# Optimization experiments

Hardware: AMD Instinct MI355X
Metric: run time of the kernel (lower is better)

Reference implementation:

```python
import jax, jax.numpy as jnp
import numpy as np

BETA = 0.0  # vcon_steps=0 -> beta=0 -> pure MAM (max+min) path


def setup_inputs() -> dict:
    key = jax.random.key(0)
    k1, k2, k3 = jax.random.split(key, 3)
    in_features, out_features, tokens = 1024, 512, 256
    x = jax.random.normal(k1, (tokens, in_features), dtype=jnp.float32)
    # torch stores weight as [out_features, in_features]
    weight = jax.random.normal(k2, (out_features, in_features), dtype=jnp.float32) * (1.0 / np.sqrt(in_features))
    bias = jax.random.normal(k3, (out_features,), dtype=jnp.float32) * 0.02
    return {"x": x, "weight": weight, "bias": bias}


def reference(x, weight, bias):
    # w: [K, N] as in the kernel (weight.T)
    w = weight.T
    # elementwise-product tensor [B, K, N]; kernel fuses this with online max/min
    prod = x[:, :, None] * w[None, :, :]
    mam = jnp.max(prod, axis=1) + jnp.min(prod, axis=1)  # [B, N]
    if BETA > 0.0:
        lin = jnp.matmul(x, w)
        out = BETA * lin + (1.0 - BETA) * mam + bias
    else:
        out = mam + bias
    return out
```

## Files before the change

kernel.cpp:

```cpp
#include <hip/hip_runtime.h>
#include <float.h>

#define B_TOK 256
#define N_OUT 512
#define K_IN  1024

#define KSPLIT 8
#define KT     (K_IN / KSPLIT)
#define BT     16
#define NT     64

__global__ __launch_bounds__(256)
void mam_stage1(const float* __restrict__ x, const float* __restrict__ w,
                float* __restrict__ pmx, float* __restrict__ pmn) {
    __shared__ float lds[10240];
    float* ws = lds;
    float* xs = lds + 8192;

    const int tid = threadIdx.x;
    const int wv  = tid >> 6;
    const int ln  = tid & 63;
    const int b0  = blockIdx.x * BT;
    const int n0  = blockIdx.y * NT;
    const int kc  = blockIdx.z * KT;

    {
        const int cb = ln & 15;
        const int u  = ln >> 4;
#pragma unroll
        for (int p = 0; p < 4; ++p) {
            const int r = 16 * wv + 4 * p + u;
            const int q = r >> 2;
            const float* src = w + (size_t)(n0 + r) * K_IN + kc;
#pragma unroll
            for (int m = 0; m < 2; ++m) {
                const int c = cb + 16 * m;
                const float4 v = *reinterpret_cast<const float4*>(src + c * 4);
                *reinterpret_cast<float4*>(&ws[r * 128 + ((c ^ q) << 2)]) = v;
            }
        }
    }
    {
        const int cb = ln & 15;
        const int u  = ln >> 4;
        const int b  = 4 * wv + u;
        const float* src = x + (size_t)(b0 + b) * K_IN + kc;
#pragma unroll
        for (int m = 0; m < 2; ++m) {
            const int c = cb + 16 * m;
            const float4 v = *reinterpret_cast<const float4*>(src + c * 4);
            *reinterpret_cast<float4*>(&xs[b * 128 + ((c ^ b) << 2)]) = v;
        }
    }
    __syncthreads();

    const int nq = ln & 15;
    const int bq = ln >> 4;

    float mx[4][4], mn[4][4];
#pragma unroll
    for (int i = 0; i < 4; ++i)
#pragma unroll
        for (int j = 0; j < 4; ++j) { mx[i][j] = -FLT_MAX; mn[i][j] = FLT_MAX; }

#pragma unroll 2
    for (int cl = 0; cl < 8; ++cl) {
        const int c = 8 * wv + cl;
        float4 wf[4], xf[4];
#pragma unroll
        for (int j = 0; j < 4; ++j)
            wf[j] = *reinterpret_cast<const float4*>(
                &ws[(4 * nq + j) * 128 + ((c ^ nq) << 2)]);
#pragma unroll
        for (int i = 0; i < 4; ++i)
            xf[i] = *reinterpret_cast<const float4*>(
                &xs[(4 * bq + i) * 128 + ((c ^ (4 * bq + i)) << 2)]);

#pragma unroll
        for (int i = 0; i < 4; ++i) {
#pragma unroll
            for (int j = 0; j < 4; ++j) {
                const float p0 = xf[i].x * wf[j].x;
                const float p1 = xf[i].y * wf[j].y;
                const float p2 = xf[i].z * wf[j].z;
                const float p3 = xf[i].w * wf[j].w;
                mx[i][j] = fmaxf(fmaxf(mx[i][j], p0), p1);
                mx[i][j] = fmaxf(fmaxf(mx[i][j], p2), p3);
                mn[i][j] = fminf(fminf(mn[i][j], p0), p1);
                mn[i][j] = fminf(fminf(mn[i][j], p2), p3);
            }
        }
    }

    __syncthreads();
    float* red = lds;
#pragma unroll
    for (int i = 0; i < 4; ++i) {
        const int ol = (4 * bq + i) * 64 + 4 * nq;
        float4 a = make_float4(mx[i][0], mx[i][1], mx[i][2], mx[i][3]);
        float4 d = make_float4(mn[i][0], mn[i][1], mn[i][2], mn[i][3]);
        *reinterpret_cast<float4*>(&red[(wv * 2 + 0) * 1024 + ol]) = a;
        *reinterpret_cast<float4*>(&red[(wv * 2 + 1) * 1024 + ol]) = d;
    }
    __syncthreads();

    {
        float4 MX = *reinterpret_cast<const float4*>(&red[0 * 1024 + tid * 4]);
        float4 MN = *reinterpret_cast<const float4*>(&red[1 * 1024 + tid * 4]);
#pragma unroll
        for (int v = 1; v < 4; ++v) {
            const float4 a = *reinterpret_cast<const float4*>(&red[(v * 2 + 0) * 1024 + tid * 4]);
            const float4 d = *reinterpret_cast<const float4*>(&red[(v * 2 + 1) * 1024 + tid * 4]);
            MX.x = fmaxf(MX.x, a.x); MX.y = fmaxf(MX.y, a.y);
            MX.z = fmaxf(MX.z, a.z); MX.w = fmaxf(MX.w, a.w);
            MN.x = fminf(MN.x, d.x); MN.y = fminf(MN.y, d.y);
            MN.z = fminf(MN.z, d.z); MN.w = fminf(MN.w, d.w);
        }
        const int bl = tid >> 4;
        const int nl = (tid & 15) * 4;
        const size_t o = ((size_t)blockIdx.z * B_TOK + b0 + bl) * N_OUT + n0 + nl;
        *reinterpret_cast<float4*>(&pmx[o]) = MX;
        *reinterpret_cast<float4*>(&pmn[o]) = MN;
    }
}

__global__ __launch_bounds__(256)
void mam_stage2(const float* __restrict__ pmx, const float* __restrict__ pmn,
                const float* __restrict__ bias, float* __restrict__ out) {
    const size_t i4 = ((size_t)blockIdx.x * 256 + threadIdx.x) * 4;
    const size_t plane = (size_t)B_TOK * N_OUT;
    float4 MX = *reinterpret_cast<const float4*>(pmx + i4);
    float4 MN = *reinterpret_cast<const float4*>(pmn + i4);
#pragma unroll
    for (int p = 1; p < KSPLIT; ++p) {
        const float4 a = *reinterpret_cast<const float4*>(pmx + (size_t)p * plane + i4);
        const float4 d = *reinterpret_cast<const float4*>(pmn + (size_t)p * plane + i4);
        MX.x = fmaxf(MX.x, a.x); MX.y = fmaxf(MX.y, a.y);
        MX.z = fmaxf(MX.z, a.z); MX.w = fmaxf(MX.w, a.w);
        MN.x = fminf(MN.x, d.x); MN.y = fminf(MN.y, d.y);
        MN.z = fminf(MN.z, d.z); MN.w = fminf(MN.w, d.w);
    }
    const float4 bb = *reinterpret_cast<const float4*>(bias + (i4 & (N_OUT - 1)));
    float4 o;
    o.x = MX.x + MN.x + bb.x; o.y = MX.y + MN.y + bb.y;
    o.z = MX.z + MN.z + bb.z; o.w = MX.w + MN.w + bb.w;
    *reinterpret_cast<float4*>(out + i4) = o;
}

__global__ __launch_bounds__(256)
void mam_simple(const float* __restrict__ x, const float* __restrict__ w,
                const float* __restrict__ bias, float* __restrict__ out) {
    const int idx = blockIdx.x * 256 + threadIdx.x;
    const int b = idx / N_OUT, n = idx % N_OUT;
    const float* xr = x + (size_t)b * K_IN;
    const float* wr = w + (size_t)n * K_IN;
    float mx = -FLT_MAX, mn = FLT_MAX;
#pragma unroll 4
    for (int k = 0; k < K_IN; k += 4) {
        const float4 xv = *reinterpret_cast<const float4*>(xr + k);
        const float4 wv = *reinterpret_cast<const float4*>(wr + k);
        const float p0 = xv.x * wv.x, p1 = xv.y * wv.y;
        const float p2 = xv.z * wv.z, p3 = xv.w * wv.w;
        mx = fmaxf(fmaxf(mx, p0), p1);
        mx = fmaxf(fmaxf(mx, p2), p3);
        mn = fminf(fminf(mn, p0), p1);
        mn = fminf(fminf(mn, p2), p3);
    }
    out[idx] = mx + mn + bias[n];
}

extern "C" void kernel_launch(void* const* d_in, const int* in_sizes, int n_in,
                              void* d_out, int out_size, void* d_ws, size_t ws_size,
                              hipStream_t stream) {
    const float* x    = (const float*)d_in[0];
    const float* w    = (const float*)d_in[1];
    const float* bias = (const float*)d_in[2];
    float* out = (float*)d_out;

    const size_t plane = (size_t)B_TOK * N_OUT;
    const size_t need  = 2 * (size_t)KSPLIT * plane * sizeof(float);

    if (ws_size >= need) {
        float* pmx = (float*)d_ws;
        float* pmn = pmx + (size_t)KSPLIT * plane;
        mam_stage1<<<dim3(B_TOK / BT, N_OUT / NT, KSPLIT), 256, 0, stream>>>(x, w, pmx, pmn);
        mam_stage2<<<(int)(plane / 4 / 256), 256, 0, stream>>>(pmx, pmn, bias, out);
    } else {
        mam_simple<<<(B_TOK * N_OUT) / 256, 256, 0, stream>>>(x, w, bias, out);
    }
}
```

Baseline: 20.92 us.

## Enlarge stage1 tile to 32x64 with 4x8 register blocking and tree reduction

Doubles the token tile per block (BT 16->32) so each thread keeps a 4x8 register tile of max/min accumulators, which raises the compute done per LDS load. It reorders the grid so the K-split index varies fastest, likely for L2 reuse of x/w, and changes the LDS swizzle. The cross-wave reduction becomes a register-blob tree merge through LDS, and only wave 0 writes the partial results. The risks are higher register pressure, half as many blocks, and idle waves during the serialized merge steps.

```diff
diff --git a/kernel.cpp b/kernel.cpp
--- a/kernel.cpp
+++ b/kernel.cpp
@@ -6,80 +6,69 @@
 #define K_IN  1024
 
 #define KSPLIT 8
-#define KT     (K_IN / KSPLIT)
-#define BT     16
+#define KT     128
+#define BT     32
 #define NT     64
 
 __global__ __launch_bounds__(256)
 void mam_stage1(const float* __restrict__ x, const float* __restrict__ w,
                 float* __restrict__ pmx, float* __restrict__ pmn) {
-    __shared__ float lds[10240];
+    __shared__ float lds[12288];
     float* ws = lds;
     float* xs = lds + 8192;
 
     const int tid = threadIdx.x;
     const int wv  = tid >> 6;
     const int ln  = tid & 63;
-    const int b0  = blockIdx.x * BT;
+    const int kc  = blockIdx.x;
     const int n0  = blockIdx.y * NT;
-    const int kc  = blockIdx.z * KT;
-
-    {
-        const int cb = ln & 15;
-        const int u  = ln >> 4;
-#pragma unroll
-        for (int p = 0; p < 4; ++p) {
-            const int r = 16 * wv + 4 * p + u;
-            const int q = r >> 2;
-            const float* src = w + (size_t)(n0 + r) * K_IN + kc;
-#pragma unroll
-            for (int m = 0; m < 2; ++m) {
-                const int c = cb + 16 * m;
-                const float4 v = *reinterpret_cast<const float4*>(src + c * 4);
-                *reinterpret_cast<float4*>(&ws[r * 128 + ((c ^ q) << 2)]) = v;
-            }
-        }
-    }
-    {
-        const int cb = ln & 15;
-        const int u  = ln >> 4;
-        const int b  = 4 * wv + u;
-        const float* src = x + (size_t)(b0 + b) * K_IN + kc;
-#pragma unroll
-        for (int m = 0; m < 2; ++m) {
-            const int c = cb + 16 * m;
-            const float4 v = *reinterpret_cast<const float4*>(src + c * 4);
-            *reinterpret_cast<float4*>(&xs[b * 128 + ((c ^ b) << 2)]) = v;
-        }
-    }
-    __syncthreads();
-
-    const int nq = ln & 15;
-    const int bq = ln >> 4;
-
-    float mx[4][4], mn[4][4];
+    const int b0  = blockIdx.z * BT;
+    const int k0  = kc * KT;
+
+#pragma unroll
+    for (int i = 0; i < 8; ++i) {
+        const int s = tid + 256 * i;
+        const int r = s >> 5, c = s & 31;
+        const float4 v = *reinterpret_cast<const float4*>(
+            w + (size_t)(n0 + r) * K_IN + k0 + 4 * c);
+        *reinterpret_cast<float4*>(&ws[r * 128 + ((c ^ ((r >> 3) & 7)) << 2)]) = v;
+    }
+#pragma unroll
+    for (int i = 0; i < 4; ++i) {
+        const int s = tid + 256 * i;
+        const int r = s >> 5, c = s & 31;
+        const float4 v = *reinterpret_cast<const float4*>(
+            x + (size_t)(b0 + r) * K_IN + k0 + 4 * c);
+        *reinterpret_cast<float4*>(&xs[r * 128 + ((c ^ ((r >> 2) & 7)) << 2)]) = v;
+    }
+    __syncthreads();
+
+    const int nq = ln & 7;
+    const int bq = ln >> 3;
+
+    float mx[4][8], mn[4][8];
 #pragma unroll
     for (int i = 0; i < 4; ++i)
 #pragma unroll
-        for (int j = 0; j < 4; ++j) { mx[i][j] = -FLT_MAX; mn[i][j] = FLT_MAX; }
+        for (int j = 0; j < 8; ++j) { mx[i][j] = -FLT_MAX; mn[i][j] = FLT_MAX; }
 
 #pragma unroll 2
-    for (int cl = 0; cl < 8; ++cl) {
-        const int c = 8 * wv + cl;
-        float4 wf[4], xf[4];
-#pragma unroll
-        for (int j = 0; j < 4; ++j)
+    for (int ci = 0; ci < 8; ++ci) {
+        const int c = 8 * wv + ci;
+        float4 wf[8], xf[4];
+#pragma unroll
+        for (int j = 0; j < 8; ++j)
             wf[j] = *reinterpret_cast<const float4*>(
-                &ws[(4 * nq + j) * 128 + ((c ^ nq) << 2)]);
+                &ws[(nq * 8 + j) * 128 + ((c ^ nq) << 2)]);
 #pragma unroll
         for (int i = 0; i < 4; ++i)
             xf[i] = *reinterpret_cast<const float4*>(
-                &xs[(4 * bq + i) * 128 + ((c ^ (4 * bq + i)) << 2)]);
+                &xs[(bq * 4 + i) * 128 + ((c ^ bq) << 2)]);
 
 #pragma unroll
         for (int i = 0; i < 4; ++i) {
 #pragma unroll
-            for (int j = 0; j < 4; ++j) {
+            for (int j = 0; j < 8; ++j) {
                 const float p0 = xf[i].x * wf[j].x;
                 const float p1 = xf[i].y * wf[j].y;
                 const float p2 = xf[i].z * wf[j].z;
@@ -91,37 +80,68 @@
             }
         }
     }
-
-    __syncthreads();
-    float* red = lds;
-#pragma unroll
-    for (int i = 0; i < 4; ++i) {
-        const int ol = (4 * bq + i) * 64 + 4 * nq;
-        float4 a = make_float4(mx[i][0], mx[i][1], mx[i][2], mx[i][3]);
-        float4 d = make_float4(mn[i][0], mn[i][1], mn[i][2], mn[i][3]);
-        *reinterpret_cast<float4*>(&red[(wv * 2 + 0) * 1024 + ol]) = a;
-        *reinterpret_cast<float4*>(&red[(wv * 2 + 1) * 1024 + ol]) = d;
-    }
-    __syncthreads();
-
-    {
-        float4 MX = *reinterpret_cast<const float4*>(&red[0 * 1024 + tid * 4]);
-        float4 MN = *reinterpret_cast<const float4*>(&red[1 * 1024 + tid * 4]);
-#pragma unroll
-        for (int v = 1; v < 4; ++v) {
-            const float4 a = *reinterpret_cast<const float4*>(&red[(v * 2 + 0) * 1024 + tid * 4]);
-            const float4 d = *reinterpret_cast<const float4*>(&red[(v * 2 + 1) * 1024 + tid * 4]);
-            MX.x = fmaxf(MX.x, a.x); MX.y = fmaxf(MX.y, a.y);
-            MX.z = fmaxf(MX.z, a.z); MX.w = fmaxf(MX.w, a.w);
-            MN.x = fminf(MN.x, d.x); MN.y = fminf(MN.y, d.y);
-            MN.z = fminf(MN.z, d.z); MN.w = fminf(MN.w, d.w);
+    __syncthreads();
+
+#define BLOB_ST(BUF, F, V) \
+    *reinterpret_cast<float4*>(&(BUF)[((F) * 64 + ln) * 4]) = (V)
+#define BLOB_LD(BUF, F) \
+    (*reinterpret_cast<const float4*>(&(BUF)[((F) * 64 + ln) * 4]))
+#define WRITE_BLOB(BUF) do {                                                      \
+    _Pragma("unroll")                                                             \
+    for (int i = 0; i < 4; ++i) {                                                 \
+        BLOB_ST(BUF, i * 2 + 0, make_float4(mx[i][0], mx[i][1], mx[i][2], mx[i][3])); \
+        BLOB_ST(BUF, i * 2 + 1, make_float4(mx[i][4], mx[i][5], mx[i][6], mx[i][7])); \
+        BLOB_ST(BUF, 8 + i * 2 + 0, make_float4(mn[i][0], mn[i][1], mn[i][2], mn[i][3])); \
+        BLOB_ST(BUF, 8 + i * 2 + 1, make_float4(mn[i][4], mn[i][5], mn[i][6], mn[i][7])); \
+    } } while (0)
+#define MERGE_BLOB(BUF) do {                                                      \
+    _Pragma("unroll")                                                             \
+    for (int i = 0; i < 4; ++i) {                                                 \
+        float4 a0 = BLOB_LD(BUF, i * 2 + 0), a1 = BLOB_LD(BUF, i * 2 + 1);        \
+        float4 d0 = BLOB_LD(BUF, 8 + i * 2 + 0), d1 = BLOB_LD(BUF, 8 + i * 2 + 1);\
+        mx[i][0] = fmaxf(mx[i][0], a0.x); mx[i][1] = fmaxf(mx[i][1], a0.y);       \
+        mx[i][2] = fmaxf(mx[i][2], a0.z); mx[i][3] = fmaxf(mx[i][3], a0.w);       \
+        mx[i][4] = fmaxf(mx[i][4], a1.x); mx[i][5] = fmaxf(mx[i][5], a1.y);       \
+        mx[i][6] = fmaxf(mx[i][6], a1.z); mx[i][7] = fmaxf(mx[i][7], a1.w);       \
+        mn[i][0] = fminf(mn[i][0], d0.x); mn[i][1] = fminf(mn[i][1], d0.y);       \
+        mn[i][2] = fminf(mn[i][2], d0.z); mn[i][3] = fminf(mn[i][3], d0.w);       \
+        mn[i][4] = fminf(mn[i][4], d1.x); mn[i][5] = fminf(mn[i][5], d1.y);       \
+        mn[i][6] = fminf(mn[i][6], d1.z); mn[i][7] = fminf(mn[i][7], d1.w);       \
+    } } while (0)
+
+    float* buf0 = lds;
+    float* buf1 = lds + 4096;
+
+    if (wv == 1) WRITE_BLOB(buf0);
+    if (wv == 3) WRITE_BLOB(buf1);
+    __syncthreads();
+    if (wv == 0) MERGE_BLOB(buf0);
+    if (wv == 2) MERGE_BLOB(buf1);
+    __syncthreads();
+    if (wv == 2) WRITE_BLOB(buf0);
+    __syncthreads();
+
+    if (wv == 0) {
+        MERGE_BLOB(buf0);
+        const size_t plane = (size_t)B_TOK * N_OUT;
+#pragma unroll
+        for (int i = 0; i < 4; ++i) {
+            const size_t o = (size_t)kc * plane
+                           + (size_t)(b0 + bq * 4 + i) * N_OUT + n0 + nq * 8;
+            *reinterpret_cast<float4*>(&pmx[o + 0]) =
+                make_float4(mx[i][0], mx[i][1], mx[i][2], mx[i][3]);
+            *reinterpret_cast<float4*>(&pmx[o + 4]) =
+                make_float4(mx[i][4], mx[i][5], mx[i][6], mx[i][7]);
+            *reinterpret_cast<float4*>(&pmn[o + 0]) =
+                make_float4(mn[i][0], mn[i][1], mn[i][2], mn[i][3]);
+            *reinterpret_cast<float4*>(&pmn[o + 4]) =
+                make_float4(mn[i][4], mn[i][5], mn[i][6], mn[i][7]);
         }
-        const int bl = tid >> 4;
-        const int nl = (tid & 15) * 4;
-        const size_t o = ((size_t)blockIdx.z * B_TOK + b0 + bl) * N_OUT + n0 + nl;
-        *reinterpret_cast<float4*>(&pmx[o]) = MX;
-        *reinterpret_cast<float4*>(&pmn[o]) = MN;
-    }
+    }
+#undef BLOB_ST
+#undef BLOB_LD
+#undef WRITE_BLOB
+#undef MERGE_BLOB
 }
 
 __global__ __launch_bounds__(256)
@@ -183,7 +203,7 @@
     if (ws_size >= need) {
         float* pmx = (float*)d_ws;
         float* pmn = pmx + (size_t)KSPLIT * plane;
-        mam_stage1<<<dim3(B_TOK / BT, N_OUT / NT, KSPLIT), 256, 0, stream>>>(x, w, pmx, pmn);
+        mam_stage1<<<dim3(KSPLIT, N_OUT / NT, B_TOK / BT), 256, 0, stream>>>(x, w, pmx, pmn);
         mam_stage2<<<(int)(plane / 4 / 256), 256, 0, stream>>>(pmx, pmn, bias, out);
     } else {
         mam_simple<<<(B_TOK * N_OUT) / 256, 256, 0, stream>>>(x, w, bias, out);
```

After: 21.29 us. Within noise of the previous version (+1.8%).
